# Performance work log

Hardware: AMD Instinct MI355X
Metric: run time of the kernel (lower is better)

The kernel has to match this reference:

```python
import jax, jax.numpy as jnp
import numpy as np

B, S, D = 4, 2048, 1024
H = 16
DK = D // H  # 64
F = 4096


def layer_norm(x, g, b, eps=1e-5):
    mu = jnp.mean(x, axis=-1, keepdims=True)
    var = jnp.mean(jnp.square(x - mu), axis=-1, keepdims=True)
    return (x - mu) * jax.lax.rsqrt(var + eps) * g + b


def setup_inputs() -> dict:
    key = jax.random.key(0)
    ks = jax.random.split(key, 12)
    s_in = 1.0 / np.sqrt(D)
    s_ff = 1.0 / np.sqrt(F)
    return {
        "x": jax.random.normal(ks[0], (B, S, D), jnp.float32),
        # per-head Q/K/V projections stacked: [H, D, DK]
        "Wq": jax.random.normal(ks[1], (H, D, DK), jnp.float32) * s_in,
        "bq": jnp.zeros((H, DK), jnp.float32),
        "Wk": jax.random.normal(ks[2], (H, D, DK), jnp.float32) * s_in,
        "bk": jnp.zeros((H, DK), jnp.float32),
        "Wv": jax.random.normal(ks[3], (H, D, DK), jnp.float32) * s_in,
        "bv": jnp.zeros((H, DK), jnp.float32),
        # output projection: [H*DK, D]
        "Wo": jax.random.normal(ks[4], (H * DK, D), jnp.float32) * s_in,
        "bo": jnp.zeros((D,), jnp.float32),
        "ln1_g": jnp.ones((D,), jnp.float32),
        "ln1_b": jnp.zeros((D,), jnp.float32),
        # FFN
        "W1": jax.random.normal(ks[5], (D, F), jnp.float32) * s_in,
        "b1": jnp.zeros((F,), jnp.float32),
        "W2": jax.random.normal(ks[6], (F, D), jnp.float32) * s_ff,
        "b2": jnp.zeros((D,), jnp.float32),
        "ln2_g": jnp.ones((D,), jnp.float32),
        "ln2_b": jnp.zeros((D,), jnp.float32),
    }


def reference(x, Wq, bq, Wk, bk, Wv, bv, Wo, bo, ln1_g, ln1_b,
              W1, b1, W2, b2, ln2_g, ln2_b):
    # --- multi-head attention (self-attention: q = k = v = x) ---
    q = jnp.einsum("bsd,hdk->bhsk", x, Wq) + bq[:, None, :]
    k = jnp.einsum("bsd,hdk->bhsk", x, Wk) + bk[:, None, :]
    v = jnp.einsum("bsd,hdk->bhsk", x, Wv) + bv[:, None, :]
    scale = 1.0 / jnp.sqrt(jnp.asarray(DK, x.dtype))
    scores = jnp.einsum("bhsk,bhtk->bhst", q, k) * scale  # [B,H,S,S]
    attn = jax.nn.softmax(scores, axis=-1)
    ctx = jnp.einsum("bhst,bhtk->bhsk", attn, v)           # [B,H,S,DK]
    # concat heads -> [B,S,H*DK], output projection
    ctx = jnp.transpose(ctx, (0, 2, 1, 3)).reshape(B, S, H * DK)
    attn_out = ctx @ Wo + bo
    # residual + post-LN (dropout is identity in eval mode)
    h = layer_norm(x + attn_out, ln1_g, ln1_b)
    # --- feed-forward (tanh activation) ---
    ff = jnp.tanh(h @ W1 + b1) @ W2 + b2
    return layer_norm(h + ff, ln2_g, ln2_b)
```

## Files before the change

kernel.cpp:

```cpp
#include <hip/hip_runtime.h>
#include <hip/hip_bf16.h>
#include <math.h>

typedef __attribute__((ext_vector_type(8))) short short8;
typedef __attribute__((ext_vector_type(4))) float f32x4;

#define NB 4
#define NS 2048
#define ND 1024
#define NH 16
#define NDK 64
#define NF 4096
#define NM (NB*NS)

#define QSCALE 0.18033688f
#define SMAX 32.0f

__device__ __forceinline__ unsigned short f2b(float f) {
  union { __hip_bfloat16 h; unsigned short u; } c;
  c.h = __float2bfloat16(f);
  return c.u;
}

__device__ __forceinline__ float b2f(unsigned short u) {
  union { float f; unsigned int i; } c;
  c.i = ((unsigned int)u) << 16;
  return c.f;
}

__device__ __forceinline__ void gload_lds16(const void* g, void* l) {
  __builtin_amdgcn_global_load_lds((const __attribute__((address_space(1))) void*)g,
                                   (__attribute__((address_space(3))) void*)l,
                                   16, 0, 0);
}

__device__ __forceinline__ float fast_tanh(float x) {
  float e = __builtin_amdgcn_exp2f(x * 2.885390082f);
  return 1.0f - 2.0f * __builtin_amdgcn_rcpf(e + 1.0f);
}


__global__ __launch_bounds__(256)
void cvt_f32_bf16(const float* __restrict__ in, unsigned short* __restrict__ out, int n4) {
  int i = blockIdx.x * 256 + threadIdx.x;
  if (i >= n4) return;
  float4 v = ((const float4*)in)[i];
  ushort4 o;
  o.x = f2b(v.x); o.y = f2b(v.y); o.z = f2b(v.z); o.w = f2b(v.w);
  ((ushort4*)out)[i] = o;
}

__global__ __launch_bounds__(256)
void transpose_generic(const float* __restrict__ src, unsigned short* __restrict__ dst,
                       int ldsrc, int lddst) {
  __shared__ float t[32][33];
  int k0 = blockIdx.x * 32, n0 = blockIdx.y * 32;
  int tx = threadIdx.x, ty = threadIdx.y;
  for (int r = ty; r < 32; r += 8)
    t[r][tx] = src[(size_t)(k0 + r) * ldsrc + n0 + tx];
  __syncthreads();
  for (int r = ty; r < 32; r += 8)
    dst[(size_t)(n0 + r) * lddst + k0 + tx] = f2b(t[tx][r]);
}

__global__ __launch_bounds__(256)
void transpose_qkv(const float* __restrict__ Wq, const float* __restrict__ Wk,
                   const float* __restrict__ Wv, unsigned short* __restrict__ dst) {
  int z = blockIdx.z, which = z / 16, h = z % 16;
  const float* src = (which == 0 ? Wq : which == 1 ? Wk : Wv) + (size_t)h * ND * NDK;
  float scale = (which == 0) ? QSCALE : 1.0f;
  unsigned short* d = dst + (size_t)(which * 1024 + h * 64) * ND;
  __shared__ float t[32][33];
  int k0 = blockIdx.x * 32, n0 = blockIdx.y * 32;
  int tx = threadIdx.x, ty = threadIdx.y;
  for (int r = ty; r < 32; r += 8)
    t[r][tx] = src[(size_t)(k0 + r) * NDK + n0 + tx];
  __syncthreads();
  for (int r = ty; r < 32; r += 8)
    d[(size_t)(n0 + r) * ND + k0 + tx] = f2b(t[tx][r] * scale);
}

__global__ __launch_bounds__(256)
void pack_bias(const float* __restrict__ bq, const float* __restrict__ bk,
               const float* __restrict__ bv, float* __restrict__ out) {
  int i = blockIdx.x * 256 + threadIdx.x;
  if (i >= 3072) return;
  float v = (i < 1024) ? bq[i] * QSCALE : (i < 2048 ? bk[i - 1024] : bv[i - 2048]);
  out[i] = v;
}

__global__ __launch_bounds__(256)
void transpose_v(const unsigned short* __restrict__ qkv, unsigned short* __restrict__ vt) {
  __shared__ unsigned short t[32][33];
  int bh = blockIdx.z; int b = bh >> 4, h = bh & 15;
  int s0 = blockIdx.x * 32;
  int d0 = blockIdx.y * 32;
  int tx = threadIdx.x, ty = threadIdx.y;
  for (int r = ty; r < 32; r += 8)
    t[r][tx] = qkv[(size_t)(b * NS + s0 + r) * 3072 + 2048 + h * 64 + d0 + tx];
  __syncthreads();
  for (int r = ty; r < 32; r += 8)
    vt[((size_t)bh * 64 + d0 + r) * NS + s0 + tx] = t[tx][r];
}


template<int EPI>
__global__ __launch_bounds__(256)
void gemm_bt(const unsigned short* __restrict__ A, const unsigned short* __restrict__ Bt,
             const float* __restrict__ bias, void* __restrict__ Cout,
             int M, int N, int K)
{
  __shared__ __align__(16) unsigned short As[2][128 * 64];
  __shared__ __align__(16) unsigned short Bs[2][128 * 64];

  const int id = blockIdx.x;
  const int xcd = id & 7;
  const int s = id >> 3;
  const int nbPerX = (N >> 7) >> 3;
  const int nb = xcd * nbPerX + (s % nbPerX);
  const int mb = s / nbPerX;
  const int n0 = nb * 128;
  const int m0 = mb * 128;

  const int tid = threadIdx.x;
  const int wave = tid >> 6, lane = tid & 63;
  const int l16 = lane & 15, lhi = lane >> 4;
  const int wr = wave >> 1, wc = wave & 1;

  const int rowL = lane >> 3;
  const int gg = (lane & 7) ^ rowL;
  const int ca = wave * 4;

  f32x4 acc[4][4] = {};

  auto STAGE = [&](int buf, int kt) {
    const int k0 = kt * 64;
#pragma unroll
    for (int c = ca; c < ca + 4; ++c) {
      gload_lds16(A + (size_t)(m0 + c * 8 + rowL) * K + (k0 + gg * 8), &As[buf][c * 512]);
      gload_lds16(Bt + (size_t)(n0 + c * 8 + rowL) * K + (k0 + gg * 8), &Bs[buf][c * 512]);
    }
  };

  auto COMPUTE = [&](int buf) {
    const char* as = (const char*)&As[buf][0];
    const char* bs = (const char*)&Bs[buf][0];
    short8 af[4][2], bf[4][2];
#pragma unroll
    for (int i = 0; i < 4; ++i) {
      const int row = wr * 64 + i * 16 + l16;
      const char* rb = as + row * 128;
#pragma unroll
      for (int ks = 0; ks < 2; ++ks)
        af[i][ks] = *(const short8*)(rb + (((ks * 4 + lhi) ^ (row & 7)) << 4));
    }
#pragma unroll
    for (int j = 0; j < 4; ++j) {
      const int row = wc * 64 + j * 16 + l16;
      const char* rb = bs + row * 128;
#pragma unroll
      for (int ks = 0; ks < 2; ++ks)
        bf[j][ks] = *(const short8*)(rb + (((ks * 4 + lhi) ^ (row & 7)) << 4));
    }
    __builtin_amdgcn_s_setprio(1);
#pragma unroll
    for (int i = 0; i < 4; ++i)
#pragma unroll
      for (int j = 0; j < 4; ++j)
#pragma unroll
        for (int ks = 0; ks < 2; ++ks)
          acc[i][j] = __builtin_amdgcn_mfma_f32_16x16x32_bf16(af[i][ks], bf[j][ks],
                                                              acc[i][j], 0, 0, 0);
    __builtin_amdgcn_s_setprio(0);
  };

  const int NT = K >> 6;
  STAGE(0, 0);
  __syncthreads();
  int cur = 0;
  for (int kt = 0; kt < NT - 1; ++kt) {
    STAGE(cur ^ 1, kt + 1);
    COMPUTE(cur);
    __syncthreads();
    cur ^= 1;
  }
  COMPUTE(cur);

#pragma unroll
  for (int i = 0; i < 4; ++i) {
    const int row = m0 + wr * 64 + i * 16 + lhi * 4;
#pragma unroll
    for (int j = 0; j < 4; ++j) {
      const int col = n0 + wc * 64 + j * 16 + l16;
      const float bv = bias[col];
#pragma unroll
      for (int r = 0; r < 4; ++r) {
        float v = acc[i][j][r] + bv;
        size_t idx = (size_t)(row + r) * N + col;
        if (EPI == 0)      ((unsigned short*)Cout)[idx] = f2b(v);
        else if (EPI == 1) ((float*)Cout)[idx] = v;
        else               ((unsigned short*)Cout)[idx] = f2b(fast_tanh(v));
      }
    }
  }
}


__global__ __launch_bounds__(512)
void attn_fwd(const unsigned short* __restrict__ qkv, const unsigned short* __restrict__ vtg,
              unsigned short* __restrict__ ctx)
{
  const int id = blockIdx.x;
  const int swz = (id & 7) * 128 + (id >> 3);
  const int qt = swz & 15;
  const int bh = swz >> 4;
  const int b = bh >> 4, h = bh & 15;
  const int row0 = b * NS + qt * 128;
  const int tid = threadIdx.x;
  const int wave = tid >> 6, lane = tid & 63;
  const int l16 = lane & 15, lhi = lane >> 4;

  __shared__ __align__(16) unsigned short Ks[2][64 * 64];
  __shared__ __align__(16) unsigned short Vs[2][64 * 64];
  __shared__ __align__(16) unsigned short Ps[8][16 * 64];

  const unsigned short* kbase = qkv + ND + (size_t)h * 64;
  const unsigned short* vbase = vtg + (size_t)bh * 64 * NS;

  const int r0 = tid >> 3;
  const int f0 = ((tid & 7) ^ (r0 & 7)) * 8;
  const int ldsb0 = wave * 512;

  short8 qf[2];
  {
    const unsigned short* qrow = qkv + (size_t)(row0 + wave * 16 + l16) * 3072 + h * 64;
    qf[0] = *(const short8*)(qrow + lhi * 8);
    qf[1] = *(const short8*)(qrow + 32 + lhi * 8);
  }

  f32x4 o[4] = {};
  float lr = 0.f;

  auto STAGE = [&](int buf, int kt) {
    const size_t kr = (size_t)(b * NS + kt * 64);
    const int kb64 = kt * 64;
    gload_lds16(kbase + (kr + r0) * 3072 + f0, &Ks[buf][ldsb0]);
    gload_lds16(vbase + (size_t)r0 * NS + kb64 + f0, &Vs[buf][ldsb0]);
  };

  auto COMPUTE = [&](int buf) {
    const char* kb = (const char*)&Ks[buf][0];
    const char* vb = (const char*)&Vs[buf][0];
    char* pb = (char*)&Ps[wave][0];

    f32x4 s[4] = {};
    __builtin_amdgcn_s_setprio(1);
#pragma unroll
    for (int c = 0; c < 2; ++c)
#pragma unroll
      for (int j = 0; j < 4; ++j) {
        const int row = j * 16 + l16;
        short8 kf = *(const short8*)(kb + row * 128 + ((c * 64 + lhi * 16) ^ ((row & 7) << 4)));
        s[j] = __builtin_amdgcn_mfma_f32_16x16x32_bf16(kf, qf[c], s[j], 0, 0, 0);
      }
    __builtin_amdgcn_s_setprio(0);

    float ls = 0.f;
#pragma unroll
    for (int j = 0; j < 4; ++j)
#pragma unroll
      for (int r = 0; r < 4; ++r) {
        float t = __builtin_amdgcn_exp2f(s[j][r] - SMAX);
        s[j][r] = t; ls += t;
      }
    lr += ls;

#pragma unroll
    for (int j = 0; j < 4; ++j)
#pragma unroll
      for (int rr = 0; rr < 2; ++rr) {
        unsigned int w = (unsigned int)f2b(s[j][2 * rr]) | ((unsigned int)f2b(s[j][2 * rr + 1]) << 16);
        *(unsigned int*)(pb + l16 * 128 + ((j * 32 + lhi * 8 + rr * 4) ^ ((l16 & 7) << 4))) = w;
      }

    __builtin_amdgcn_s_setprio(1);
#pragma unroll
    for (int c = 0; c < 2; ++c) {
      short8 pf = *(const short8*)(pb + l16 * 128 + ((c * 64 + lhi * 16) ^ ((l16 & 7) << 4)));
#pragma unroll
      for (int j = 0; j < 4; ++j) {
        const int row = j * 16 + l16;
        short8 vf = *(const short8*)(vb + row * 128 + ((c * 64 + lhi * 16) ^ ((row & 7) << 4)));
        o[j] = __builtin_amdgcn_mfma_f32_16x16x32_bf16(pf, vf, o[j], 0, 0, 0);
      }
    }
    __builtin_amdgcn_s_setprio(0);
  };

  STAGE(0, 0);
  __syncthreads();
  int cur = 0;
  for (int kt = 0; kt < NS / 64 - 1; ++kt) {
    STAGE(cur ^ 1, kt + 1);
    COMPUTE(cur);
    __syncthreads();
    cur ^= 1;
  }
  COMPUTE(cur);

  float t = lr;
  t += __shfl_xor(t, 16);
  t += __shfl_xor(t, 32);
  float rinv[4];
#pragma unroll
  for (int r = 0; r < 4; ++r) rinv[r] = 1.0f / __shfl(t, lhi * 4 + r);
#pragma unroll
  for (int j = 0; j < 4; ++j)
#pragma unroll
    for (int r = 0; r < 4; ++r) {
      const int row = row0 + wave * 16 + lhi * 4 + r;
      ctx[(size_t)row * ND + h * 64 + j * 16 + l16] = f2b(o[j][r] * rinv[r]);
    }
}


template<int MODE>
__global__ __launch_bounds__(256)
void ln_fused(const void* xa_, const void* xb_,
              const float* g, const float* beta, void* out_)
{
  const int row = blockIdx.x;
  const int tid = threadIdx.x;
  const int wave = tid >> 6, lane = tid & 63;
  __shared__ float r1[4], r2[4];

  float a0, a1, a2, a3;
  if (MODE == 0) {
    float4 a = ((const float4*)((const float*)xa_ + (size_t)row * ND))[tid];
    a0 = a.x; a1 = a.y; a2 = a.z; a3 = a.w;
  } else {
    ushort4 a = ((const ushort4*)((const unsigned short*)xa_ + (size_t)row * ND))[tid];
    a0 = b2f(a.x); a1 = b2f(a.y); a2 = b2f(a.z); a3 = b2f(a.w);
  }
  ushort4 bu = ((const ushort4*)((const unsigned short*)xb_ + (size_t)row * ND))[tid];
  float v0 = a0 + b2f(bu.x), v1 = a1 + b2f(bu.y), v2 = a2 + b2f(bu.z), v3 = a3 + b2f(bu.w);

  float sm = v0 + v1 + v2 + v3;
#pragma unroll
  for (int d = 1; d < 64; d <<= 1) sm += __shfl_xor(sm, d);
  if (lane == 0) r1[wave] = sm;
  __syncthreads();
  const float mu = (r1[0] + r1[1] + r1[2] + r1[3]) * (1.0f / ND);
  const float d0 = v0 - mu, d1 = v1 - mu, d2 = v2 - mu, d3 = v3 - mu;
  float vs = d0 * d0 + d1 * d1 + d2 * d2 + d3 * d3;
#pragma unroll
  for (int d = 1; d < 64; d <<= 1) vs += __shfl_xor(vs, d);
  if (lane == 0) r2[wave] = vs;
  __syncthreads();
  const float var = (r2[0] + r2[1] + r2[2] + r2[3]) * (1.0f / ND);
  const float inv = rsqrtf(var + 1e-5f);
  float4 gg = ((const float4*)g)[tid];
  float4 bb = ((const float4*)beta)[tid];
  float o0 = d0 * inv * gg.x + bb.x;
  float o1 = d1 * inv * gg.y + bb.y;
  float o2 = d2 * inv * gg.z + bb.z;
  float o3 = d3 * inv * gg.w + bb.w;
  if (MODE == 0) {
    ushort4 w; w.x = f2b(o0); w.y = f2b(o1); w.z = f2b(o2); w.w = f2b(o3);
    ((ushort4*)((unsigned short*)out_ + (size_t)row * ND))[tid] = w;
  } else {
    float4 ov; ov.x = o0; ov.y = o1; ov.z = o2; ov.w = o3;
    ((float4*)((float*)out_ + (size_t)row * ND))[tid] = ov;
  }
}


extern "C" void kernel_launch(void* const* d_in, const int* in_sizes, int n_in,
                              void* d_out, int out_size, void* d_ws, size_t ws_size,
                              hipStream_t stream)
{
  (void)in_sizes; (void)n_in; (void)out_size; (void)ws_size;
  const float* x   = (const float*)d_in[0];
  const float* Wq  = (const float*)d_in[1];
  const float* bq  = (const float*)d_in[2];
  const float* Wk  = (const float*)d_in[3];
  const float* bk  = (const float*)d_in[4];
  const float* Wv  = (const float*)d_in[5];
  const float* bv  = (const float*)d_in[6];
  const float* Wo  = (const float*)d_in[7];
  const float* bo  = (const float*)d_in[8];
  const float* g1  = (const float*)d_in[9];
  const float* be1 = (const float*)d_in[10];
  const float* W1  = (const float*)d_in[11];
  const float* b1  = (const float*)d_in[12];
  const float* W2  = (const float*)d_in[13];
  const float* b2  = (const float*)d_in[14];
  const float* g2  = (const float*)d_in[15];
  const float* be2 = (const float*)d_in[16];

  char* ws = (char*)d_ws;
  const size_t MB = 1ull << 20;
  unsigned short* x_bf  = (unsigned short*)(ws);
  unsigned short* vtg   = (unsigned short*)(ws);
  unsigned short* qkv   = (unsigned short*)(ws + 16 * MB);
  unsigned short* aout  = (unsigned short*)(ws + 16 * MB);
  unsigned short* ff1   = (unsigned short*)(ws);
  unsigned short* ctx   = (unsigned short*)(ws + 64 * MB);
  unsigned short* h_bf  = (unsigned short*)(ws + 64 * MB);
  unsigned short* Wqkvt = (unsigned short*)(ws + 80 * MB);
  unsigned short* Wot   = (unsigned short*)(ws + 86 * MB);
  unsigned short* W1t   = (unsigned short*)(ws + 88 * MB);
  unsigned short* W2t   = (unsigned short*)(ws + 96 * MB);
  float*          bqkv  = (float*)(ws + 104 * MB);
  unsigned short* ffout = (unsigned short*)(ws + 105 * MB);

  cvt_f32_bf16<<<NM * ND / 4 / 256, 256, 0, stream>>>(x, x_bf, NM * ND / 4);
  transpose_qkv<<<dim3(32, 2, 48), dim3(32, 8), 0, stream>>>(Wq, Wk, Wv, Wqkvt);
  transpose_generic<<<dim3(32, 32), dim3(32, 8), 0, stream>>>(Wo, Wot, 1024, 1024);
  transpose_generic<<<dim3(32, 128), dim3(32, 8), 0, stream>>>(W1, W1t, 4096, 1024);
  transpose_generic<<<dim3(128, 32), dim3(32, 8), 0, stream>>>(W2, W2t, 1024, 4096);
  pack_bias<<<12, 256, 0, stream>>>(bq, bk, bv, bqkv);

  gemm_bt<0><<<(NM / 128) * (3072 / 128), 256, 0, stream>>>(x_bf, Wqkvt, bqkv, qkv, NM, 3072, 1024);
  transpose_v<<<dim3(64, 2, 64), dim3(32, 8), 0, stream>>>(qkv, vtg);
  attn_fwd<<<1024, 512, 0, stream>>>(qkv, vtg, ctx);
  gemm_bt<0><<<(NM / 128) * (1024 / 128), 256, 0, stream>>>(ctx, Wot, bo, aout, NM, 1024, 1024);
  ln_fused<0><<<NM, 256, 0, stream>>>(x, aout, g1, be1, h_bf);
  gemm_bt<2><<<(NM / 128) * (4096 / 128), 256, 0, stream>>>(h_bf, W1t, b1, ff1, NM, 4096, 1024);
  gemm_bt<0><<<(NM / 128) * (1024 / 128), 256, 0, stream>>>(ff1, W2t, b2, ffout, NM, 1024, 4096);
  ln_fused<1><<<NM, 256, 0, stream>>>(h_bf, ffout, g2, be2, (float*)d_out);
}
```

Before: 458.9 us.

## Enlarge GEMM tiles to 256x128 with 512 threads and unroll double buffering

```diff
diff --git a/kernel.cpp b/kernel.cpp
--- a/kernel.cpp
+++ b/kernel.cpp
@@ -105,22 +105,21 @@
 
 
 template<int EPI>
-__global__ __launch_bounds__(256)
+__global__ __launch_bounds__(512, 1)
 void gemm_bt(const unsigned short* __restrict__ A, const unsigned short* __restrict__ Bt,
              const float* __restrict__ bias, void* __restrict__ Cout,
              int M, int N, int K)
 {
-  __shared__ __align__(16) unsigned short As[2][128 * 64];
+  __shared__ __align__(16) unsigned short As[2][256 * 64];
   __shared__ __align__(16) unsigned short Bs[2][128 * 64];
 
+  const int nwg = gridDim.x;
   const int id = blockIdx.x;
-  const int xcd = id & 7;
-  const int s = id >> 3;
-  const int nbPerX = (N >> 7) >> 3;
-  const int nb = xcd * nbPerX + (s % nbPerX);
-  const int mb = s / nbPerX;
+  const int swz = (id & 7) * (nwg >> 3) + (id >> 3);
+  const int nbx = N >> 7;
+  const int mb = swz / nbx, nb = swz % nbx;
+  const int m0 = mb * 256;
   const int n0 = nb * 128;
-  const int m0 = mb * 128;
 
   const int tid = threadIdx.x;
   const int wave = tid >> 6, lane = tid & 63;
@@ -129,17 +128,17 @@
 
   const int rowL = lane >> 3;
   const int gg = (lane & 7) ^ rowL;
-  const int ca = wave * 4;
 
   f32x4 acc[4][4] = {};
 
   auto STAGE = [&](int buf, int kt) {
     const int k0 = kt * 64;
 #pragma unroll
-    for (int c = ca; c < ca + 4; ++c) {
+    for (int c = wave * 4; c < wave * 4 + 4; ++c)
       gload_lds16(A + (size_t)(m0 + c * 8 + rowL) * K + (k0 + gg * 8), &As[buf][c * 512]);
+#pragma unroll
+    for (int c = wave * 2; c < wave * 2 + 2; ++c)
       gload_lds16(Bt + (size_t)(n0 + c * 8 + rowL) * K + (k0 + gg * 8), &Bs[buf][c * 512]);
-    }
   };
 
   auto COMPUTE = [&](int buf) {
@@ -177,14 +176,14 @@
   const int NT = K >> 6;
   STAGE(0, 0);
   __syncthreads();
-  int cur = 0;
-  for (int kt = 0; kt < NT - 1; ++kt) {
-    STAGE(cur ^ 1, kt + 1);
-    COMPUTE(cur);
+  for (int j = 0; j < NT; j += 2) {
+    STAGE(1, j + 1);
+    COMPUTE(0);
     __syncthreads();
-    cur ^= 1;
-  }
-  COMPUTE(cur);
+    if (j + 2 < NT) STAGE(0, j + 2);
+    COMPUTE(1);
+    __syncthreads();
+  }
 
 #pragma unroll
   for (int i = 0; i < 4; ++i) {
@@ -299,14 +298,14 @@
 
   STAGE(0, 0);
   __syncthreads();
-  int cur = 0;
-  for (int kt = 0; kt < NS / 64 - 1; ++kt) {
-    STAGE(cur ^ 1, kt + 1);
-    COMPUTE(cur);
+  for (int kt = 0; kt < NS / 64; kt += 2) {
+    STAGE(1, kt + 1);
+    COMPUTE(0);
     __syncthreads();
-    cur ^= 1;
-  }
-  COMPUTE(cur);
+    if (kt + 2 < NS / 64) STAGE(0, kt + 2);
+    COMPUTE(1);
+    __syncthreads();
+  }
 
   float t = lr;
   t += __shfl_xor(t, 16);
@@ -421,12 +420,12 @@
   transpose_generic<<<dim3(128, 32), dim3(32, 8), 0, stream>>>(W2, W2t, 1024, 4096);
   pack_bias<<<12, 256, 0, stream>>>(bq, bk, bv, bqkv);
 
-  gemm_bt<0><<<(NM / 128) * (3072 / 128), 256, 0, stream>>>(x_bf, Wqkvt, bqkv, qkv, NM, 3072, 1024);
+  gemm_bt<0><<<(NM / 256) * (3072 / 128), 512, 0, stream>>>(x_bf, Wqkvt, bqkv, qkv, NM, 3072, 1024);
   transpose_v<<<dim3(64, 2, 64), dim3(32, 8), 0, stream>>>(qkv, vtg);
   attn_fwd<<<1024, 512, 0, stream>>>(qkv, vtg, ctx);
-  gemm_bt<0><<<(NM / 128) * (1024 / 128), 256, 0, stream>>>(ctx, Wot, bo, aout, NM, 1024, 1024);
+  gemm_bt<0><<<(NM / 256) * (1024 / 128), 512, 0, stream>>>(ctx, Wot, bo, aout, NM, 1024, 1024);
   ln_fused<0><<<NM, 256, 0, stream>>>(x, aout, g1, be1, h_bf);
-  gemm_bt<2><<<(NM / 128) * (4096 / 128), 256, 0, stream>>>(h_bf, W1t, b1, ff1, NM, 4096, 1024);
-  gemm_bt<0><<<(NM / 128) * (1024 / 128), 256, 0, stream>>>(ff1, W2t, b2, ffout, NM, 1024, 4096);
+  gemm_bt<2><<<(NM / 256) * (4096 / 128), 512, 0, stream>>>(h_bf, W1t, b1, ff1, NM, 4096, 1024);
+  gemm_bt<0><<<(NM / 256) * (1024 / 128), 512, 0, stream>>>(ff1, W2t, b2, ffout, NM, 1024, 4096);
   ln_fused<1><<<NM, 256, 0, stream>>>(h_bf, ffout, g2, be2, (float*)d_out);
 }
```

Result: faster. 441.7 us (-3.7%).
